# Optimization experiments

Measured on AMD Instinct MI355X. Metric: run time of the kernel, lower is better.

## Reference

```python
import jax, jax.numpy as jnp
import numpy as np

DIM = 4096
N_HEADS = 32
N_KV_HEADS = 8
HEAD_DIM = DIM // N_HEADS      # 128
N_REP = N_HEADS // N_KV_HEADS  # 4
B, S = 2, 2048
THETA = 10000.0


def _rope_tables(seq_len, head_dim):
    # standard llama2.c freqs: [1, S, 1, head_dim//2]
    freqs = 1.0 / (THETA ** (np.arange(0, head_dim, 2, dtype=np.float32) / head_dim))
    t = np.arange(seq_len, dtype=np.float32)
    ang = np.outer(t, freqs)  # [S, head_dim//2]
    cos = jnp.asarray(np.cos(ang))[None, :, None, :]
    sin = jnp.asarray(np.sin(ang))[None, :, None, :]
    return cos, sin


def setup_inputs() -> dict:
    key = jax.random.key(0)
    ks = jax.random.split(key, 5)
    x = jax.random.normal(ks[0], (B, S, DIM), dtype=jnp.float32)
    freqs_cos, freqs_sin = _rope_tables(S, HEAD_DIM)
    scale = 1.0 / np.sqrt(DIM)
    wq = jax.random.normal(ks[1], (DIM, N_HEADS * HEAD_DIM), dtype=jnp.float32) * scale
    wk = jax.random.normal(ks[2], (DIM, N_KV_HEADS * HEAD_DIM), dtype=jnp.float32) * scale
    wv = jax.random.normal(ks[3], (DIM, N_KV_HEADS * HEAD_DIM), dtype=jnp.float32) * scale
    wo = jax.random.normal(ks[4], (N_HEADS * HEAD_DIM, DIM), dtype=jnp.float32) * scale
    return {"x": x, "freqs_cos": freqs_cos, "freqs_sin": freqs_sin,
            "wq": wq, "wk": wk, "wv": wv, "wo": wo}


def _apply_rotary(t, cos, sin):
    # t: [B, S, H, head_dim]; cos/sin: [1, S, 1, head_dim//2]
    b, s, h, d = t.shape
    tr = t.reshape(b, s, h, d // 2, 2)
    t_r, t_i = tr[..., 0], tr[..., 1]
    out_r = t_r * cos - t_i * sin
    out_i = t_r * sin + t_i * cos
    return jnp.stack([out_r, out_i], axis=-1).reshape(b, s, h, d)


def reference(x, freqs_cos, freqs_sin, wq, wk, wv, wo):
    b, s, _ = x.shape
    q = (x @ wq).reshape(b, s, N_HEADS, HEAD_DIM)
    k = (x @ wk).reshape(b, s, N_KV_HEADS, HEAD_DIM)
    v = (x @ wv).reshape(b, s, N_KV_HEADS, HEAD_DIM)
    q = _apply_rotary(q, freqs_cos, freqs_sin)
    k = _apply_rotary(k, freqs_cos, freqs_sin)
    # GQA: repeat kv heads to match q heads
    k = jnp.repeat(k, N_REP, axis=2)  # [b, s, H, hd]
    v = jnp.repeat(v, N_REP, axis=2)
    # NOTE: source calls SDPA with attn_mask=None and no is_causal -> non-causal
    scores = jnp.einsum('bqhd,bkhd->bhqk', q, k) / jnp.sqrt(
        jnp.asarray(HEAD_DIM, dtype=q.dtype))
    attn = jax.nn.softmax(scores, axis=-1)
    out = jnp.einsum('bhqk,bkhd->bqhd', attn, v)
    out = out.reshape(b, s, N_HEADS * HEAD_DIM)
    return out @ wo
```

## Files before the change

### kernel.cpp

```cpp
#include <hip/hip_runtime.h>
#include <cstdint>


typedef __attribute__((ext_vector_type(8))) short short8;
typedef __attribute__((ext_vector_type(4))) float f32x4;
typedef __attribute__((ext_vector_type(16))) float f32x16;

__device__ __forceinline__ float bf2f(unsigned short u) {
  union { unsigned int i; float f; } v; v.i = ((unsigned int)u) << 16; return v.f;
}
__device__ __forceinline__ unsigned short f2bf(float f) {
  union { float f; unsigned int i; } v; v.f = f;
  unsigned int r = v.i + 0x7fffu + ((v.i >> 16) & 1u);
  return (unsigned short)(r >> 16);
}

__device__ __forceinline__ void gload_lds16(const void* g, void* lds) {
  __builtin_amdgcn_global_load_lds(
      (const __attribute__((address_space(1))) unsigned int*)g,
      (__attribute__((address_space(3))) unsigned int*)lds, 16, 0, 0);
}

__device__ __forceinline__ unsigned int cvtpk_bf16(float lo, float hi) {
  unsigned int r;
  asm("v_cvt_pk_bf16_f32 %0, %1, %2" : "=v"(r) : "v"(lo), "v"(hi));
  return r;
}
__device__ __forceinline__ void pl32swap(unsigned int& a, unsigned int& b) {
  asm("v_permlane32_swap_b32 %0, %1" : "+v"(a), "+v"(b));
}


__global__ __launch_bounds__(256) void cast_bf16(const float* __restrict__ src,
                                                 unsigned short* __restrict__ dst) {
  size_t i = (size_t)blockIdx.x * 256 + threadIdx.x;
  float4 v = ((const float4*)src)[i];
  ushort4 o; o.x = f2bf(v.x); o.y = f2bf(v.y); o.z = f2bf(v.z); o.w = f2bf(v.w);
  ((ushort4*)dst)[i] = o;
}

__global__ __launch_bounds__(256) void transpose_cast(const float* __restrict__ src,
                                                      unsigned short* __restrict__ dst,
                                                      int R, int C) {
  __shared__ float tile[32][33];
  int c0 = blockIdx.x * 32, r0 = blockIdx.y * 32;
  int tx = threadIdx.x & 31, ty = threadIdx.x >> 5;
#pragma unroll
  for (int j = 0; j < 4; ++j)
    tile[ty + j * 8][tx] = src[(size_t)(r0 + ty + j * 8) * C + c0 + tx];
  __syncthreads();
#pragma unroll
  for (int j = 0; j < 4; ++j)
    dst[(size_t)(c0 + ty + j * 8) * R + r0 + tx] = f2bf(tile[tx][ty + j * 8]);
}

__global__ __launch_bounds__(256) void rope_k(unsigned short* __restrict__ qkv,
                                              const float* __restrict__ cosT,
                                              const float* __restrict__ sinT) {
  int idx = blockIdx.x * 256 + threadIdx.x;
  int t = idx / 640;
  int cb = (idx - t * 640) * 8;
  int s = t & 2047;
  int j0 = (cb & 127) >> 1;
  unsigned short* p = qkv + (size_t)t * 6144 + cb;
  uint4 u = *(const uint4*)p;
  float4 c4 = *(const float4*)&cosT[s * 64 + j0];
  float4 s4 = *(const float4*)&sinT[s * 64 + j0];
  auto rot = [](unsigned int& uu, float c, float sn) {
    float re = bf2f((unsigned short)(uu & 0xffffu));
    float im = bf2f((unsigned short)(uu >> 16));
    float nr = re * c - im * sn;
    float ni = re * sn + im * c;
    uu = (unsigned int)f2bf(nr) | ((unsigned int)f2bf(ni) << 16);
  };
  rot(u.x, c4.x, s4.x); rot(u.y, c4.y, s4.y);
  rot(u.z, c4.z, s4.z); rot(u.w, c4.w, s4.w);
  *(uint4*)p = u;
}


#define GBAR() asm volatile("s_barrier" ::: "memory")
#define GVM6() asm volatile("s_waitcnt vmcnt(6)" ::: "memory")
#define GVM4() asm volatile("s_waitcnt vmcnt(4)" ::: "memory")
#define GHINT() asm volatile("s_waitcnt lgkmcnt(8)" ::: "memory")

#define GLDA(buf, mh)                                                                   \
  do {                                                                                  \
    _Pragma("unroll") for (int m_ = 0; m_ < 4; ++m_)                                    \
    _Pragma("unroll") for (int ks_ = 0; ks_ < 2; ++ks_)                                 \
      a[m_][ks_] = *(const short8*)&smem[buf][0]                                        \
          [(wm * 128 + (mh) * 64 + m_ * 16 + lr) * 64 + (((ks_ * 4 + lg) ^ (lr & 7)) << 3)]; \
  } while (0)

#define GLDB(bf_, buf, nh)                                                              \
  do {                                                                                  \
    _Pragma("unroll") for (int n_ = 0; n_ < 2; ++n_)                                    \
    _Pragma("unroll") for (int ks_ = 0; ks_ < 2; ++ks_)                                 \
      bf_[n_][ks_] = *(const short8*)&smem[buf][1]                                      \
          [(wn * 64 + (nh) * 32 + n_ * 16 + lr) * 64 + (((ks_ * 4 + lg) ^ (lr & 7)) << 3)]; \
  } while (0)

#define GMM(bf_, mh, nh)                                                                \
  do {                                                                                  \
    __builtin_amdgcn_s_setprio(1);                                                      \
    _Pragma("unroll") for (int ks_ = 0; ks_ < 2; ++ks_)                                 \
    _Pragma("unroll") for (int m_ = 0; m_ < 4; ++m_)                                    \
    _Pragma("unroll") for (int n_ = 0; n_ < 2; ++n_)                                    \
      acc[(mh) * 4 + m_][(nh) * 2 + n_] = __builtin_amdgcn_mfma_f32_16x16x32_bf16(      \
          a[m_][ks_], bf_[n_][ks_], acc[(mh) * 4 + m_][(nh) * 2 + n_], 0, 0, 0);        \
    __builtin_amdgcn_s_setprio(0);                                                      \
  } while (0)

#define GSTG(half, buf, tile)                                                           \
  do {                                                                                  \
    _Pragma("unroll") for (int t2_ = 0; t2_ < 2; ++t2_)                                 \
      gload_lds16(srcp[half][t2_] + ((size_t)(tile) << 6),                              \
                  &smem[buf][(half) >> 1][dsto[half][t2_]]);                            \
  } while (0)

template <typename OutT>
__device__ __forceinline__ void gemm256_body(const unsigned short* __restrict__ A,
                                             const unsigned short* __restrict__ B,
                                             OutT* __restrict__ C, int K, int ldc,
                                             unsigned short (*smem)[2][16384]) {
  const int bid = blockIdx.x;
  const int xcd = bid & 7, ii = bid >> 3;
  const int mt = (xcd & 3) * 4 + (ii & 3);
  const int nt = (xcd >> 2) * 8 + (ii >> 2);
  const int m0 = mt * 256, n0 = nt * 256;
  const int tid = threadIdx.x, w = tid >> 6, l = tid & 63;
  const int wm = w >> 2, wn = w & 3;
  const int lr = l & 15, lg = l >> 4;
  const int NT = K >> 6;

  const int lsub = l >> 3, lgr = l & 7;
  const int sg = (lgr ^ lsub) << 3;
  const unsigned short* srcp[4][2];
  int dsto[4][2];
#pragma unroll
  for (int t2 = 0; t2 < 2; ++t2) {
    int lb = t2 * 64 + w * 8;
    int pa0 = (lb & 63) + ((lb >> 6) << 7);
    int pb0 = (lb & 31) + ((lb >> 5) << 6);
    srcp[0][t2] = A + (size_t)(m0 + pa0 + lsub) * K + sg;       dsto[0][t2] = pa0 * 64;
    srcp[1][t2] = A + (size_t)(m0 + pa0 + 64 + lsub) * K + sg;  dsto[1][t2] = (pa0 + 64) * 64;
    srcp[2][t2] = B + (size_t)(n0 + pb0 + lsub) * K + sg;       dsto[2][t2] = pb0 * 64;
    srcp[3][t2] = B + (size_t)(n0 + pb0 + 32 + lsub) * K + sg;  dsto[3][t2] = (pb0 + 32) * 64;
  }

  f32x4 acc[8][4] = {};
  short8 a[4][2], b0f[2][2], b1f[2][2];

  GSTG(0, 0, 0); GSTG(2, 0, 0); GSTG(3, 0, 0); GSTG(1, 0, 0);
  GSTG(0, 1, 1); GSTG(2, 1, 1); GSTG(3, 1, 1);
  GVM6();
  GBAR();

  for (int t = 0; t < NT / 2; ++t) {
    const int t1 = 2 * t + 1;
    const int t2a = (2 * t + 2 < NT) ? 2 * t + 2 : NT - 1;
    const int t2b = (2 * t + 3 < NT) ? 2 * t + 3 : NT - 1;
    GLDA(0, 0); GLDB(b0f, 0, 0);
    GSTG(1, 1, t1);
    GHINT();
    GBAR(); GMM(b0f, 0, 0); GBAR();
    GLDB(b1f, 0, 1);
    GSTG(0, 0, t2a);
    GBAR(); GMM(b1f, 0, 1); GBAR();
    GLDA(0, 1);
    GSTG(2, 0, t2a);
    GBAR(); GMM(b0f, 1, 0); GBAR();
    GSTG(3, 0, t2a);
    GBAR(); GMM(b1f, 1, 1); GVM6(); GBAR();
    GLDA(1, 0); GLDB(b0f, 1, 0);
    GSTG(1, 0, t2a);
    GHINT();
    GBAR(); GMM(b0f, 0, 0); GBAR();
    GLDB(b1f, 1, 1);
    GSTG(0, 1, t2b);
    GBAR(); GMM(b1f, 0, 1); GBAR();
    GLDA(1, 1);
    GSTG(2, 1, t2b);
    GBAR(); GMM(b0f, 1, 0); GBAR();
    GSTG(3, 1, t2b);
    GBAR(); GMM(b1f, 1, 1); GVM6(); GBAR();
  }

#pragma unroll
  for (int m = 0; m < 8; ++m)
#pragma unroll
    for (int n = 0; n < 4; ++n)
#pragma unroll
      for (int r = 0; r < 4; ++r) {
        int row = m0 + wm * 128 + m * 16 + lg * 4 + r;
        int col = n0 + wn * 64 + n * 16 + lr;
        float v = acc[m][n][r];
        if constexpr (sizeof(OutT) == 2)
          C[(size_t)row * ldc + col] = (OutT)f2bf(v);
        else
          C[(size_t)row * ldc + col] = v;
      }
}

__global__ __launch_bounds__(512) void gemm_qproj(const unsigned short* __restrict__ A,
                                                  const unsigned short* __restrict__ B,
                                                  unsigned short* __restrict__ C,
                                                  int K, int ldc) {
  __shared__ unsigned short smem[2][2][16384];
  gemm256_body<unsigned short>(A, B, C, K, ldc, smem);
}

__global__ __launch_bounds__(512) void gemm_oproj(const unsigned short* __restrict__ A,
                                                  const unsigned short* __restrict__ B,
                                                  float* __restrict__ C,
                                                  int K, int ldc) {
  __shared__ unsigned short smem[2][2][16384];
  gemm256_body<float>(A, B, C, K, ldc, smem);
}


#define KLDA(buf)                                                                       \
  do {                                                                                  \
    _Pragma("unroll") for (int m_ = 0; m_ < 4; ++m_)                                    \
    _Pragma("unroll") for (int ks_ = 0; ks_ < 2; ++ks_)                                 \
      a2[m_][ks_] = *(const short8*)&As2[buf]                                           \
          [(wm * 64 + m_ * 16 + lr) * 64 + (((ks_ * 4 + lg) ^ (lr & 7)) << 3)];         \
  } while (0)

#define KLDB(bf_, buf, nh)                                                              \
  do {                                                                                  \
    _Pragma("unroll") for (int n_ = 0; n_ < 2; ++n_)                                    \
    _Pragma("unroll") for (int ks_ = 0; ks_ < 2; ++ks_)                                 \
      bf_[n_][ks_] = *(const short8*)&Bs2[buf]                                          \
          [(wn * 64 + (nh) * 32 + n_ * 16 + lr) * 64 + (((ks_ * 4 + lg) ^ (lr & 7)) << 3)]; \
  } while (0)

#define KMM(bf_, nh)                                                                    \
  do {                                                                                  \
    __builtin_amdgcn_s_setprio(1);                                                      \
    _Pragma("unroll") for (int ks_ = 0; ks_ < 2; ++ks_)                                 \
    _Pragma("unroll") for (int m_ = 0; m_ < 4; ++m_)                                    \
    _Pragma("unroll") for (int n_ = 0; n_ < 2; ++n_)                                    \
      acc[m_][(nh) * 2 + n_] = __builtin_amdgcn_mfma_f32_16x16x32_bf16(                 \
          a2[m_][ks_], bf_[n_][ks_], acc[m_][(nh) * 2 + n_], 0, 0, 0);                  \
    __builtin_amdgcn_s_setprio(0);                                                      \
  } while (0)

#define KSTGA(buf, tile)                                                                \
  do {                                                                                  \
    _Pragma("unroll") for (int t2_ = 0; t2_ < 2; ++t2_)                                 \
      gload_lds16(srcA[t2_] + ((size_t)(tile) << 6), &As2[buf][dstA[t2_]]);             \
  } while (0)
#define KSTGB0(buf, tile)                                                               \
  do {                                                                                  \
    _Pragma("unroll") for (int t2_ = 0; t2_ < 2; ++t2_)                                 \
      gload_lds16(srcB0[t2_] + ((size_t)(tile) << 6), &Bs2[buf][dstB0[t2_]]);           \
  } while (0)
#define KSTGB1(buf, tile)                                                               \
  do {                                                                                  \
    _Pragma("unroll") for (int t2_ = 0; t2_ < 2; ++t2_)                                 \
      gload_lds16(srcB1[t2_] + ((size_t)(tile) << 6), &Bs2[buf][dstB1[t2_]]);           \
  } while (0)

__global__ __launch_bounds__(512) void gemm_kvproj(const unsigned short* __restrict__ A,
                                                   const unsigned short* __restrict__ B,
                                                   unsigned short* __restrict__ C,
                                                   unsigned short* __restrict__ vt,
                                                   int K, int ldc) {
  __shared__ unsigned short As2[2][8192];
  __shared__ unsigned short Bs2[2][16384];
  const int bid = blockIdx.x;
  const int xcd = bid & 7, ii = bid >> 3;
  const int mt = (xcd & 3) * 8 + (ii & 7);
  const int nt = (xcd >> 2) * 4 + (ii >> 3);
  const int m0 = mt * 128, n0 = nt * 256;
  const int tid = threadIdx.x, w = tid >> 6, l = tid & 63;
  const int wm = w >> 2, wn = w & 3;
  const int lr = l & 15, lg = l >> 4;
  const int NT = K >> 6;

  const int lsub = l >> 3, lgr = l & 7;
  const int sg = (lgr ^ lsub) << 3;
  const unsigned short* srcA[2];  int dstA[2];
  const unsigned short* srcB0[2]; int dstB0[2];
  const unsigned short* srcB1[2]; int dstB1[2];
#pragma unroll
  for (int t2 = 0; t2 < 2; ++t2) {
    int ra = t2 * 64 + w * 8;
    srcA[t2] = A + (size_t)(m0 + ra + lsub) * K + sg;            dstA[t2] = ra * 64;
    int lb = t2 * 64 + w * 8;
    int pb0 = (lb & 31) + ((lb >> 5) << 6);
    srcB0[t2] = B + (size_t)(n0 + pb0 + lsub) * K + sg;          dstB0[t2] = pb0 * 64;
    srcB1[t2] = B + (size_t)(n0 + pb0 + 32 + lsub) * K + sg;     dstB1[t2] = (pb0 + 32) * 64;
  }

  f32x4 acc[4][4] = {};
  short8 a2[4][2], bb0[2][2], bb1[2][2];

  KSTGA(0, 0); KSTGB0(0, 0); KSTGB1(0, 0);
  KSTGA(1, 1); KSTGB0(1, 1);
  GVM4();
  GBAR();

  for (int t = 0; t < NT / 2; ++t) {
    const int t1 = 2 * t + 1;
    const int t2a = (2 * t + 2 < NT) ? 2 * t + 2 : NT - 1;
    const int t2b = (2 * t + 3 < NT) ? 2 * t + 3 : NT - 1;
    KLDA(0); KLDB(bb0, 0, 0);
    KSTGB1(1, t1);
    GHINT();
    GBAR(); KMM(bb0, 0); GBAR();
    KLDB(bb1, 0, 1);
    KSTGA(0, t2a); KSTGB0(0, t2a);
    GBAR(); KMM(bb1, 1); GVM4(); GBAR();
    KLDA(1); KLDB(bb0, 1, 0);
    KSTGB1(0, t2a);
    GHINT();
    GBAR(); KMM(bb0, 0); GBAR();
    KLDB(bb1, 1, 1);
    KSTGA(1, t2b); KSTGB0(1, t2b);
    GBAR(); KMM(bb1, 1); GVM4(); GBAR();
  }

  if (n0 >= 1024) {
#pragma unroll
    for (int m = 0; m < 4; ++m)
#pragma unroll
      for (int n = 0; n < 4; ++n) {
        const int col = n0 + wn * 64 + n * 16 + lr;
        const int kvh = (col - 1024) >> 7, d = (col - 1024) & 127;
        const int row0 = m0 + wm * 64 + m * 16 + lg * 4;
        const int bb = row0 >> 11, tok = row0 & 2047;
        ushort4 o;
        o.x = f2bf(acc[m][n][0]); o.y = f2bf(acc[m][n][1]);
        o.z = f2bf(acc[m][n][2]); o.w = f2bf(acc[m][n][3]);
        *(ushort4*)&vt[(size_t)((bb * 8 + kvh) * 128 + d) * 2048 + tok] = o;
      }
  } else {
#pragma unroll
    for (int m = 0; m < 4; ++m)
#pragma unroll
      for (int n = 0; n < 4; ++n)
#pragma unroll
        for (int r = 0; r < 4; ++r) {
          int row = m0 + wm * 64 + m * 16 + lg * 4 + r;
          int col = n0 + wn * 64 + n * 16 + lr;
          C[(size_t)row * ldc + col] = f2bf(acc[m][n][r]);
        }
  }
}


__global__ __launch_bounds__(256, 2) void attn_k(const unsigned short* __restrict__ qkv,
                                                 const unsigned short* __restrict__ vt,
                                                 unsigned short* __restrict__ ctx) {
  __shared__ unsigned short Ks[2][64 * 128];
  __shared__ unsigned short Vs[2][128 * 64];
  const int bid = blockIdx.x;
  const int xcd = bid & 7, idx = bid >> 3;
  const int kvg = xcd * 2 + (idx >> 6);
  const int hg = (idx >> 4) & 3;
  const int qt = idx & 15;
  const int b = kvg >> 3, kvh = kvg & 7, h = kvh * 4 + hg;
  const int w = threadIdx.x >> 6, l = threadIdx.x & 63;
  const int lc = l & 31, hi = l >> 5;
  const size_t tok0 = (size_t)b * 2048;
  const int q0 = qt * 128 + w * 32;
  const float C2 = 0.12751744516557944f;

  const unsigned short* ksrc[4];
  const unsigned short* vsrc[4];
#pragma unroll
  for (int i = 0; i < 4; ++i) {
    int L = w * 256 + i * 64 + l;
    int krow = L >> 4, kc = L & 15;
    ksrc[i] = qkv + (tok0 + krow) * 6144 + 4096 + kvh * 128 + ((kc ^ (krow & 7)) << 3);
    int vrow = L >> 3, vc = L & 7;
    vsrc[i] = vt + (size_t)(kvg * 128 + vrow) * 2048 + ((vc ^ (vrow & 7)) << 3);
  }
  const int ldsBase = (w * 256) * 8;

  auto stage = [&](int bufi, int kv0s) {
#pragma unroll
    for (int i = 0; i < 4; ++i)
      gload_lds16(ksrc[i] + (size_t)kv0s * 6144, &Ks[bufi][ldsBase + i * 512]);
#pragma unroll
    for (int i = 0; i < 4; ++i)
      gload_lds16(vsrc[i] + kv0s, &Vs[bufi][ldsBase + i * 512]);
  };

  const unsigned short* Qb = qkv + (tok0 + q0 + lc) * 6144 + h * 128 + hi * 8;
  short8 qf[8];
#pragma unroll
  for (int dc = 0; dc < 8; ++dc) qf[dc] = *(const short8*)(Qb + dc * 16);

  f32x16 acc[4] = {};
  float lsum = 0.f;

  stage(0, 0);
  __syncthreads();

  int buf = 0;
  const int swz = (lc & 7) << 3;
  for (int kt = 0; kt < 32; ++kt) {
    if (kt < 31) stage(buf ^ 1, (kt + 1) * 64);
    f32x16 s0 = {}, s1 = {};
    __builtin_amdgcn_s_setprio(1);
#pragma unroll
    for (int dc = 0; dc < 8; ++dc) {
      int cidx = ((dc * 2 + hi) << 3) ^ swz;
      short8 kf0 = *(const short8*)&Ks[buf][lc * 128 + cidx];
      short8 kf1 = *(const short8*)&Ks[buf][(lc + 32) * 128 + cidx];
      s0 = __builtin_amdgcn_mfma_f32_32x32x16_bf16(kf0, qf[dc], s0, 0, 0, 0);
      s1 = __builtin_amdgcn_mfma_f32_32x32x16_bf16(kf1, qf[dc], s1, 0, 0, 0);
    }
    __builtin_amdgcn_s_setprio(0);
    float p[32];
#pragma unroll
    for (int r = 0; r < 16; ++r) p[r] = __builtin_amdgcn_exp2f(s0[r] * C2);
#pragma unroll
    for (int r = 0; r < 16; ++r) p[16 + r] = __builtin_amdgcn_exp2f(s1[r] * C2);
#pragma unroll
    for (int r = 0; r < 32; ++r) lsum += p[r];
    short8 pa[4];
#pragma unroll
    for (int g = 0; g < 4; ++g) {
      unsigned int c0 = cvtpk_bf16(p[g * 8 + 0], p[g * 8 + 1]);
      unsigned int c1 = cvtpk_bf16(p[g * 8 + 2], p[g * 8 + 3]);
      unsigned int c2 = cvtpk_bf16(p[g * 8 + 4], p[g * 8 + 5]);
      unsigned int c3 = cvtpk_bf16(p[g * 8 + 6], p[g * 8 + 7]);
      pl32swap(c0, c2);
      pl32swap(c1, c3);
      union { unsigned int u[4]; short8 v; } t;
      t.u[0] = c0; t.u[1] = c1; t.u[2] = c2; t.u[3] = c3;
      pa[g] = t.v;
    }
    __builtin_amdgcn_s_setprio(1);
#pragma unroll
    for (int dt = 0; dt < 4; ++dt) {
#pragma unroll
      for (int ks = 0; ks < 4; ++ks) {
        short8 vf = *(const short8*)&Vs[buf][(dt * 32 + lc) * 64 + ((((ks * 2 + hi) << 3) ^ swz))];
        acc[dt] = __builtin_amdgcn_mfma_f32_32x32x16_bf16(pa[ks], vf, acc[dt], 0, 0, 0);
      }
    }
    __builtin_amdgcn_s_setprio(0);
    __syncthreads();
    buf ^= 1;
  }
  lsum += __shfl_xor(lsum, 32, 64);
  float rl = 1.0f / lsum;
#pragma unroll
  for (int r = 0; r < 16; ++r) {
    int crow = (r & 3) + 8 * (r >> 2) + 4 * hi;
    float rlr = __shfl(rl, crow, 64);
    unsigned short* cp = ctx + (tok0 + q0 + crow) * 4096 + h * 128 + lc;
#pragma unroll
    for (int dt = 0; dt < 4; ++dt) cp[dt * 32] = f2bf(acc[dt][r] * rlr);
  }
}


extern "C" void kernel_launch(void* const* d_in, const int* in_sizes, int n_in,
                              void* d_out, int out_size, void* d_ws, size_t ws_size,
                              hipStream_t stream) {
  const float* x  = (const float*)d_in[0];
  const float* fc = (const float*)d_in[1];
  const float* fs = (const float*)d_in[2];
  const float* wq = (const float*)d_in[3];
  const float* wk = (const float*)d_in[4];
  const float* wv = (const float*)d_in[5];
  const float* wo = (const float*)d_in[6];
  float* out = (float*)d_out;
  char* ws = (char*)d_ws;

  constexpr size_t SZ_WQKVT = (size_t)6144 * 4096 * 2;
  constexpr size_t SZ_WOT   = (size_t)4096 * 4096 * 2;
  constexpr size_t SZ_QKV   = (size_t)4096 * 6144 * 2;
  constexpr size_t SZ_VT    = (size_t)16 * 128 * 2048 * 2;

  unsigned short* wqkvT = (unsigned short*)ws;
  unsigned short* woT   = (unsigned short*)(ws + SZ_WQKVT);
  unsigned short* qkv   = (unsigned short*)(ws + SZ_WQKVT + SZ_WOT);
  unsigned short* vt    = (unsigned short*)(ws + SZ_WQKVT + SZ_WOT + SZ_QKV);
  unsigned short* xbf   = (unsigned short*)(ws + SZ_WQKVT + SZ_WOT + SZ_QKV + SZ_VT);
  unsigned short* ctx   = xbf;

  cast_bf16<<<16384, 256, 0, stream>>>(x, xbf);
  transpose_cast<<<dim3(128, 128), 256, 0, stream>>>(wq, wqkvT, 4096, 4096);
  transpose_cast<<<dim3(32, 128), 256, 0, stream>>>(wk, wqkvT + (size_t)4096 * 4096, 4096, 1024);
  transpose_cast<<<dim3(32, 128), 256, 0, stream>>>(wv, wqkvT + (size_t)5120 * 4096, 4096, 1024);
  transpose_cast<<<dim3(128, 128), 256, 0, stream>>>(wo, woT, 4096, 4096);

  gemm_qproj<<<256, 512, 0, stream>>>(xbf, wqkvT, qkv, 4096, 6144);
  gemm_kvproj<<<256, 512, 0, stream>>>(xbf, wqkvT + (size_t)4096 * 4096, qkv + 4096, vt, 4096, 6144);
  rope_k<<<10240, 256, 0, stream>>>(qkv, fc, fs);
  attn_k<<<1024, 256, 0, stream>>>(qkv, vt, ctx);
  gemm_oproj<<<256, 512, 0, stream>>>(ctx, woT, out, 4096, 4096);
}
```

Baseline: 512.2 us.

## Fuse Q rotary into attention load and enlarge attention blocks to 512 threads

```diff
diff --git a/kernel.cpp b/kernel.cpp
--- a/kernel.cpp
+++ b/kernel.cpp
@@ -54,15 +54,15 @@
     dst[(size_t)(c0 + ty + j * 8) * R + r0 + tx] = f2bf(tile[tx][ty + j * 8]);
 }
 
-__global__ __launch_bounds__(256) void rope_k(unsigned short* __restrict__ qkv,
-                                              const float* __restrict__ cosT,
-                                              const float* __restrict__ sinT) {
+__global__ __launch_bounds__(256) void rope_kk(unsigned short* __restrict__ qkv,
+                                               const float* __restrict__ cosT,
+                                               const float* __restrict__ sinT) {
   int idx = blockIdx.x * 256 + threadIdx.x;
-  int t = idx / 640;
-  int cb = (idx - t * 640) * 8;
+  int t = idx >> 7;
+  int cb = (idx & 127) * 8;
   int s = t & 2047;
   int j0 = (cb & 127) >> 1;
-  unsigned short* p = qkv + (size_t)t * 6144 + cb;
+  unsigned short* p = qkv + (size_t)t * 6144 + 4096 + cb;
   uint4 u = *(const uint4*)p;
   float4 c4 = *(const float4*)&cosT[s * 64 + j0];
   float4 s4 = *(const float4*)&sinT[s * 64 + j0];
@@ -351,48 +351,66 @@
 }
 
 
-__global__ __launch_bounds__(256, 2) void attn_k(const unsigned short* __restrict__ qkv,
+__global__ __launch_bounds__(512, 4) void attn_k(const unsigned short* __restrict__ qkv,
                                                  const unsigned short* __restrict__ vt,
+                                                 const float* __restrict__ fc,
+                                                 const float* __restrict__ fs,
                                                  unsigned short* __restrict__ ctx) {
   __shared__ unsigned short Ks[2][64 * 128];
   __shared__ unsigned short Vs[2][128 * 64];
   const int bid = blockIdx.x;
   const int xcd = bid & 7, idx = bid >> 3;
-  const int kvg = xcd * 2 + (idx >> 6);
-  const int hg = (idx >> 4) & 3;
-  const int qt = idx & 15;
+  const int kvg = xcd * 2 + (idx >> 5);
+  const int hg = (idx >> 3) & 3;
+  const int qt = idx & 7;
   const int b = kvg >> 3, kvh = kvg & 7, h = kvh * 4 + hg;
   const int w = threadIdx.x >> 6, l = threadIdx.x & 63;
   const int lc = l & 31, hi = l >> 5;
   const size_t tok0 = (size_t)b * 2048;
-  const int q0 = qt * 128 + w * 32;
+  const int q0 = qt * 256 + w * 32;
   const float C2 = 0.12751744516557944f;
 
-  const unsigned short* ksrc[4];
-  const unsigned short* vsrc[4];
-#pragma unroll
-  for (int i = 0; i < 4; ++i) {
-    int L = w * 256 + i * 64 + l;
+  const unsigned short* ksrc[2];
+  const unsigned short* vsrc[2];
+#pragma unroll
+  for (int i = 0; i < 2; ++i) {
+    int L = w * 128 + i * 64 + l;
     int krow = L >> 4, kc = L & 15;
     ksrc[i] = qkv + (tok0 + krow) * 6144 + 4096 + kvh * 128 + ((kc ^ (krow & 7)) << 3);
     int vrow = L >> 3, vc = L & 7;
     vsrc[i] = vt + (size_t)(kvg * 128 + vrow) * 2048 + ((vc ^ (vrow & 7)) << 3);
   }
-  const int ldsBase = (w * 256) * 8;
+  const int ldsBase = w * 1024;
 
   auto stage = [&](int bufi, int kv0s) {
 #pragma unroll
-    for (int i = 0; i < 4; ++i)
+    for (int i = 0; i < 2; ++i)
       gload_lds16(ksrc[i] + (size_t)kv0s * 6144, &Ks[bufi][ldsBase + i * 512]);
 #pragma unroll
-    for (int i = 0; i < 4; ++i)
+    for (int i = 0; i < 2; ++i)
       gload_lds16(vsrc[i] + kv0s, &Vs[bufi][ldsBase + i * 512]);
   };
 
   const unsigned short* Qb = qkv + (tok0 + q0 + lc) * 6144 + h * 128 + hi * 8;
+  const int s = q0 + lc;
   short8 qf[8];
 #pragma unroll
-  for (int dc = 0; dc < 8; ++dc) qf[dc] = *(const short8*)(Qb + dc * 16);
+  for (int dc = 0; dc < 8; ++dc) {
+    uint4 raw = *(const uint4*)(Qb + dc * 16);
+    float4 c4 = *(const float4*)&fc[s * 64 + dc * 8 + hi * 4];
+    float4 s4 = *(const float4*)&fs[s * 64 + dc * 8 + hi * 4];
+    auto rotw = [](unsigned int uu, float c, float sn) -> unsigned int {
+      float re = bf2f((unsigned short)(uu & 0xffffu));
+      float im = bf2f((unsigned short)(uu >> 16));
+      return cvtpk_bf16(re * c - im * sn, re * sn + im * c);
+    };
+    union { unsigned int u[4]; short8 v; } t;
+    t.u[0] = rotw(raw.x, c4.x, s4.x);
+    t.u[1] = rotw(raw.y, c4.y, s4.y);
+    t.u[2] = rotw(raw.z, c4.z, s4.z);
+    t.u[3] = rotw(raw.w, c4.w, s4.w);
+    qf[dc] = t.v;
+  }
 
   f32x16 acc[4] = {};
   float lsum = 0.f;
@@ -494,7 +512,7 @@
 
   gemm_qproj<<<256, 512, 0, stream>>>(xbf, wqkvT, qkv, 4096, 6144);
   gemm_kvproj<<<256, 512, 0, stream>>>(xbf, wqkvT + (size_t)4096 * 4096, qkv + 4096, vt, 4096, 6144);
-  rope_k<<<10240, 256, 0, stream>>>(qkv, fc, fs);
-  attn_k<<<1024, 256, 0, stream>>>(qkv, vt, ctx);
+  rope_kk<<<2048, 256, 0, stream>>>(qkv, fc, fs);
+  attn_k<<<512, 512, 0, stream>>>(qkv, vt, fc, fs, ctx);
   gemm_oproj<<<256, 512, 0, stream>>>(ctx, woT, out, 4096, 4096);
 }
```

New measurement: 1.059 ms. 107% more time.
